# Kernel optimization log

Hardware: AMD Instinct MI355X
Metric: run time of the kernel (lower is better)

Reference implementation:

```python
import jax, jax.numpy as jnp
import numpy as np

IN_FEATURES = 4096
OUT_FEATURES = 4096
BANDWIDTH = min(IN_FEATURES, OUT_FEATURES) // 8  # 512, as in the torch default


def band_indices(n_out, n_in, bw):
    """Vectorized equivalent of BandMatrix.create_band_indices (COO row/col lists)."""
    i = np.arange(n_out)
    lo = np.maximum(0, i - bw)
    hi = np.minimum(n_in, i + bw + 1)
    counts = hi - lo
    total = int(counts.sum())
    rows = np.repeat(i, counts)
    start = np.cumsum(counts) - counts  # offset of each row's first entry
    cols = np.arange(total) - np.repeat(start, counts) + np.repeat(lo, counts)
    return rows.astype(np.int32), cols.astype(np.int32)


def setup_inputs() -> dict:
    key = jax.random.key(0)
    kx, kw = jax.random.split(key)
    rows_np, cols_np = band_indices(OUT_FEATURES, IN_FEATURES, BANDWIDTH)
    nnz = rows_np.shape[0]  # 3935744
    x = jax.random.normal(kx, (4, 2048, IN_FEATURES), dtype=jnp.float32)
    W_values = jax.random.normal(kw, (nnz,), dtype=jnp.float32)
    bias = jnp.zeros((OUT_FEATURES,), dtype=jnp.float32)
    return {
        "x": x,
        "W_values": W_values,
        "bias": bias,
        "rows": jnp.asarray(rows_np),
        "cols": jnp.asarray(cols_np),
    }


def reference(x, W_values, bias, rows, cols):
    # Densify banded COO weight [out, in] (matches sparse_coo_tensor().to_dense()).
    W = jnp.zeros((OUT_FEATURES, IN_FEATURES), dtype=W_values.dtype).at[rows, cols].set(W_values)
    # x: [B, S, in] @ W.T: [in, out] -> [B, S, out]
    out = jnp.einsum('bsi,oi->bso', x, W) + bias
    return out
```

## Files before the change

### kernel.cpp

```cpp
#include <hip/hip_runtime.h>
#include <stdint.h>

#define IN_F  4096
#define OUT_F 4096
#define BW    512
#define BM    256
#define BN    256
#define BK    32
#define WB2   1280

typedef __bf16 bf16x8 __attribute__((ext_vector_type(8)));
typedef float  f32x4  __attribute__((ext_vector_type(4)));

__device__ __forceinline__ int band_start(int o) {
    if (o <= 512)  return o * 513 + ((o * (o - 1)) >> 1);
    if (o <= 3584) return 393472 + (o - 512) * 1025;
    const int d = o - 3584;
    return 3542272 + (((1024 + 4609 - o) * d) >> 1);
}

__device__ __forceinline__ uint16_t f32_to_bf16(float f) {
    uint32_t u = __builtin_bit_cast(uint32_t, f);
    u += 0x7FFFu + ((u >> 16) & 1u);
    return (uint16_t)(u >> 16);
}

__global__ __launch_bounds__(256) void cvt_x(const float* __restrict__ x,
                                             uint16_t* __restrict__ xb, int n4) {
    const int stride = gridDim.x * 256;
    for (int i = blockIdx.x * 256 + threadIdx.x; i < n4; i += stride) {
        const float4 v = reinterpret_cast<const float4*>(x)[i];
        const uint32_t lo = (uint32_t)f32_to_bf16(v.x) | ((uint32_t)f32_to_bf16(v.y) << 16);
        const uint32_t hi = (uint32_t)f32_to_bf16(v.z) | ((uint32_t)f32_to_bf16(v.w) << 16);
        reinterpret_cast<uint2*>(xb)[i] = make_uint2(lo, hi);
    }
}

__global__ __launch_bounds__(256) void cvt_w(const float* __restrict__ wv,
                                             uint16_t* __restrict__ wd) {
    const int o = blockIdx.y;
    const int j = blockIdx.x * 256 + threadIdx.x;
    const int i = (o & ~(BM - 1)) - BW + j;
    uint16_t v = 0;
    if (i >= o - BW && i <= o + BW && i >= 0 && i < IN_F) {
        const int lo = (o > BW) ? (o - BW) : 0;
        v = f32_to_bf16(wv[band_start(o) + (i - lo)]);
    }
    wd[o * WB2 + j] = v;
}

__global__ __launch_bounds__(512, 2) void band_gemm_8p(
    const uint16_t* __restrict__ xb,
    const uint16_t* __restrict__ wd,
    const float* __restrict__ bias,
    float* __restrict__ out)
{
    __shared__ __align__(128) uint8_t lds[131072];

    const int id  = blockIdx.x;
    const int cpx = gridDim.x >> 3;
    const int wg  = (id & 7) * cpx + (id >> 3);
    const int bx  = wg & 15;
    const int by  = wg >> 4;
    const int brow = by * BM;
    const int bcol = bx * BN;

    const int wlo    = bcol - BW;
    const int kstart = wlo > 0 ? wlo : 0;
    const int kend   = (bcol + BN + BW) < IN_F ? (bcol + BN + BW) : IN_F;
    const int nt     = (kend - kstart) >> 5;
    const int j0     = kstart - wlo;

    const int tid  = threadIdx.x;
    const int w    = tid >> 6;
    const int lane = tid & 63;
    const int ln   = lane & 15;
    const int kc   = lane >> 4;
    const int wm   = w >> 2;
    const int wn   = w & 3;

    const int srow = tid >> 2;
    const int scs  = (tid & 3) ^ ((srow >> 1) & 3);
    const uint16_t* sA0 = xb + (size_t)(brow + srow) * IN_F + kstart + scs * 8;
    const uint16_t* sA1 = sA0 + (size_t)128 * IN_F;
    const uint16_t* sB0 = wd + (size_t)(bcol + srow) * WB2 + j0 + scs * 8;
    const uint16_t* sB1 = sB0 + (size_t)128 * WB2;

    const int swz  = (kc ^ ((ln >> 1) & 3)) << 4;
    const int aoff = ((wm << 7) + ln) << 6;
    const int boff = 16384 + (((wn << 6) + ln) << 6);

#define GLOAD(srcp, dst_off)                                                             \
    __builtin_amdgcn_global_load_lds(                                                    \
        (const __attribute__((address_space(1))) uint32_t*)(srcp),                       \
        (__attribute__((address_space(3))) uint32_t*)(lds + (dst_off) + (w << 10)),      \
        16, 0, 0)

    f32x4 acc[8][4] = {};

    #pragma unroll
    for (int tt = 0; tt < 3; ++tt) {
        GLOAD(sA0 + tt * 32, tt * 32768 + 0);
        GLOAD(sA1 + tt * 32, tt * 32768 + 8192);
        GLOAD(sB0 + tt * 32, tt * 32768 + 16384);
        GLOAD(sB1 + tt * 32, tt * 32768 + 24576);
    }
    asm volatile("s_waitcnt vmcnt(8)" ::: "memory");
    __builtin_amdgcn_s_barrier();

    for (int t = 0; t < nt; ++t) {
        const int cur = (t & 3) << 15;
        const int pr  = ((t + 3) & 3) << 15;
        const int ts  = (t + 3 < nt ? t + 3 : nt - 1) * 32;

        bf16x8 af[8];
        #pragma unroll
        for (int a = 0; a < 8; ++a)
            af[a] = *(const bf16x8*)(lds + cur + aoff + a * 1024 + swz);
        bf16x8 bf0 = *(const bf16x8*)(lds + cur + boff + 0 * 1024 + swz);
        bf16x8 bf1 = *(const bf16x8*)(lds + cur + boff + 1 * 1024 + swz);
        GLOAD(sA0 + ts, pr + 0);
        GLOAD(sA1 + ts, pr + 8192);
        asm volatile("" ::: "memory");
        __builtin_amdgcn_s_barrier();
        __builtin_amdgcn_s_setprio(1);
        #pragma unroll
        for (int a = 0; a < 8; ++a) {
            acc[a][0] = __builtin_amdgcn_mfma_f32_16x16x32_bf16(af[a], bf0, acc[a][0], 0, 0, 0);
            acc[a][1] = __builtin_amdgcn_mfma_f32_16x16x32_bf16(af[a], bf1, acc[a][1], 0, 0, 0);
        }
        __builtin_amdgcn_s_setprio(0);
        asm volatile("" ::: "memory");
        __builtin_amdgcn_s_barrier();

        bf16x8 bf2 = *(const bf16x8*)(lds + cur + boff + 2 * 1024 + swz);
        bf16x8 bf3 = *(const bf16x8*)(lds + cur + boff + 3 * 1024 + swz);
        GLOAD(sB0 + ts, pr + 16384);
        GLOAD(sB1 + ts, pr + 24576);
        asm volatile("s_waitcnt vmcnt(8)" ::: "memory");
        __builtin_amdgcn_s_barrier();
        __builtin_amdgcn_s_setprio(1);
        #pragma unroll
        for (int a = 0; a < 8; ++a) {
            acc[a][2] = __builtin_amdgcn_mfma_f32_16x16x32_bf16(af[a], bf2, acc[a][2], 0, 0, 0);
            acc[a][3] = __builtin_amdgcn_mfma_f32_16x16x32_bf16(af[a], bf3, acc[a][3], 0, 0, 0);
        }
        __builtin_amdgcn_s_setprio(0);
        asm volatile("" ::: "memory");
        __builtin_amdgcn_s_barrier();
    }
#undef GLOAD

    asm volatile("s_waitcnt vmcnt(0)" ::: "memory");

    const int ocol = bcol + (wn << 6) + ln;
    float bsv[4];
    #pragma unroll
    for (int b = 0; b < 4; ++b) bsv[b] = bias[ocol + b * 16];

    #pragma unroll
    for (int a = 0; a < 8; ++a) {
        #pragma unroll
        for (int q = 0; q < 4; ++q) {
            const int row = brow + (wm << 7) + a * 16 + (kc << 2) + q;
            float* po = out + (size_t)row * OUT_F + ocol;
            #pragma unroll
            for (int b = 0; b < 4; ++b)
                po[b * 16] = acc[a][b][q] + bsv[b];
        }
    }
}

__global__ __launch_bounds__(256) void band_gemm_f32(
    const float* __restrict__ x, const float* __restrict__ wv,
    const float* __restrict__ bias, float* __restrict__ out, int M)
{
    __shared__ float Xs[128][33];
    __shared__ float Ws[32][130];
    const int tid = threadIdx.x;
    const int tx = tid & 15, ty = tid >> 4;
    const int bcol = blockIdx.x * 128, brow = blockIdx.y * 128;
    const int klo = (bcol >= BW) ? (bcol - BW) : 0;
    const int khi = min(IN_F, bcol + 128 + BW);
    float acc[8][8];
    #pragma unroll
    for (int a = 0; a < 8; ++a)
        #pragma unroll
        for (int b = 0; b < 8; ++b) acc[a][b] = 0.f;
    const int xc4 = (tid & 7) * 4, xr0 = tid >> 3;
    const int wc = tid & 31, wr0 = tid >> 5;
    for (int k0 = klo; k0 < khi; k0 += 32) {
        #pragma unroll
        for (int p = 0; p < 4; ++p) {
            const int r = xr0 + 32 * p;
            const float4 v = *reinterpret_cast<const float4*>(&x[(size_t)(brow + r) * IN_F + (k0 + xc4)]);
            Xs[r][xc4 + 0] = v.x; Xs[r][xc4 + 1] = v.y; Xs[r][xc4 + 2] = v.z; Xs[r][xc4 + 3] = v.w;
        }
        const int i = k0 + wc;
        #pragma unroll
        for (int p = 0; p < 16; ++p) {
            const int r = wr0 + 8 * p;
            const int o = bcol + r;
            const int lo = (o >= BW) ? (o - BW) : 0;
            float v = 0.f;
            if (i >= o - BW && i <= o + BW) v = wv[band_start(o) + (i - lo)];
            Ws[wc][r] = v;
        }
        __syncthreads();
        #pragma unroll
        for (int k = 0; k < 32; ++k) {
            float am[8];
            #pragma unroll
            for (int a = 0; a < 8; ++a) am[a] = Xs[ty * 8 + a][k];
            float bo[8];
            #pragma unroll
            for (int b = 0; b < 4; ++b) { bo[b] = Ws[k][tx * 4 + b]; bo[4 + b] = Ws[k][tx * 4 + 64 + b]; }
            #pragma unroll
            for (int a = 0; a < 8; ++a)
                #pragma unroll
                for (int b = 0; b < 8; ++b) acc[a][b] = fmaf(am[a], bo[b], acc[a][b]);
        }
        __syncthreads();
    }
    #pragma unroll
    for (int a = 0; a < 8; ++a) {
        const size_t row = (size_t)(brow + ty * 8 + a);
        #pragma unroll
        for (int b = 0; b < 4; ++b) {
            out[row * OUT_F + bcol + tx * 4 + b]      = acc[a][b]     + bias[bcol + tx * 4 + b];
            out[row * OUT_F + bcol + tx * 4 + 64 + b] = acc[a][4 + b] + bias[bcol + tx * 4 + 64 + b];
        }
    }
}

extern "C" void kernel_launch(void* const* d_in, const int* in_sizes, int n_in,
                              void* d_out, int out_size, void* d_ws, size_t ws_size,
                              hipStream_t stream) {
    const float* x    = (const float*)d_in[0];
    const float* wv   = (const float*)d_in[1];
    const float* bias = (const float*)d_in[2];
    float* out        = (float*)d_out;

    const int M = in_sizes[0] / IN_F;
    const size_t xb_bytes = (size_t)M * IN_F * 2;
    const size_t wd_bytes = (size_t)OUT_F * WB2 * 2;

    if (ws_size >= xb_bytes + wd_bytes && (M % BM) == 0) {
        uint16_t* xb  = (uint16_t*)d_ws;
        uint16_t* wdp = (uint16_t*)((uint8_t*)d_ws + xb_bytes);
        cvt_x<<<2048, 256, 0, stream>>>(x, xb, M * IN_F / 4);
        cvt_w<<<dim3(WB2 / 256, OUT_F), 256, 0, stream>>>(wv, wdp);
        band_gemm_8p<<<(M / BM) * (OUT_F / BN), 512, 0, stream>>>(xb, wdp, bias, out);
    } else {
        dim3 grid(OUT_F / 128, M / 128);
        band_gemm_f32<<<grid, 256, 0, stream>>>(x, wv, bias, out, M);
    }
}
```

Baseline: 150.9 us.

## Retile band GEMM to 128x256 tiles with BK=64 triple-buffered pipeline

Shrinks the block tile from 256x256 to 128x256 and doubles the K step to 64, using three 48KB LDS buffers with a two-stage prefetch in place of four 32KB buffers. The grid doubles (more workgroups, 2 per CU still allowed), there are half as many K iterations per tile, and each iteration has a single barrier instead of several. It also changes the LDS swizzle to an 8-way XOR for 128-byte rows. In exchange, A-operand reuse per block drops (more weight traffic per output), and each wave holds a 4x4 accumulator set instead of 8x4.

```diff
diff --git a/kernel.cpp b/kernel.cpp
--- a/kernel.cpp
+++ b/kernel.cpp
@@ -4,10 +4,11 @@
 #define IN_F  4096
 #define OUT_F 4096
 #define BW    512
-#define BM    256
+#define TN    256
+#define WB2   1280
+#define BM    128
 #define BN    256
-#define BK    32
-#define WB2   1280
+#define BUFSZ 49152
 
 typedef __bf16 bf16x8 __attribute__((ext_vector_type(8)));
 typedef float  f32x4  __attribute__((ext_vector_type(4)));
@@ -40,7 +41,7 @@
                                              uint16_t* __restrict__ wd) {
     const int o = blockIdx.y;
     const int j = blockIdx.x * 256 + threadIdx.x;
-    const int i = (o & ~(BM - 1)) - BW + j;
+    const int i = (o & ~(TN - 1)) - BW + j;
     uint16_t v = 0;
     if (i >= o - BW && i <= o + BW && i >= 0 && i < IN_F) {
         const int lo = (o > BW) ? (o - BW) : 0;
@@ -49,13 +50,13 @@
     wd[o * WB2 + j] = v;
 }
 
-__global__ __launch_bounds__(512, 2) void band_gemm_8p(
+__global__ __launch_bounds__(512, 2) void band_gemm_v3(
     const uint16_t* __restrict__ xb,
     const uint16_t* __restrict__ wd,
     const float* __restrict__ bias,
     float* __restrict__ out)
 {
-    __shared__ __align__(128) uint8_t lds[131072];
+    __shared__ __align__(128) uint8_t lds[3 * BUFSZ];
 
     const int id  = blockIdx.x;
     const int cpx = gridDim.x >> 3;
@@ -63,12 +64,12 @@
     const int bx  = wg & 15;
     const int by  = wg >> 4;
     const int brow = by * BM;
-    const int bcol = bx * BN;
+    const int bcol = bx * TN;
 
     const int wlo    = bcol - BW;
     const int kstart = wlo > 0 ? wlo : 0;
-    const int kend   = (bcol + BN + BW) < IN_F ? (bcol + BN + BW) : IN_F;
-    const int nt     = (kend - kstart) >> 5;
+    const int kend   = (bcol + TN + BW) < IN_F ? (bcol + TN + BW) : IN_F;
+    const int nt     = (kend - kstart) >> 6;
     const int j0     = kstart - wlo;
 
     const int tid  = threadIdx.x;
@@ -79,16 +80,10 @@
     const int wm   = w >> 2;
     const int wn   = w & 3;
 
-    const int srow = tid >> 2;
-    const int scs  = (tid & 3) ^ ((srow >> 1) & 3);
-    const uint16_t* sA0 = xb + (size_t)(brow + srow) * IN_F + kstart + scs * 8;
-    const uint16_t* sA1 = sA0 + (size_t)128 * IN_F;
-    const uint16_t* sB0 = wd + (size_t)(bcol + srow) * WB2 + j0 + scs * 8;
-    const uint16_t* sB1 = sB0 + (size_t)128 * WB2;
-
-    const int swz  = (kc ^ ((ln >> 1) & 3)) << 4;
-    const int aoff = ((wm << 7) + ln) << 6;
-    const int boff = 16384 + (((wn << 6) + ln) << 6);
+    const int srow = tid >> 3;
+    const int csrc = (tid & 7) ^ (srow & 7);
+    const uint16_t* aSrc = xb + (size_t)(brow + srow) * IN_F + kstart + csrc * 8;
+    const uint16_t* bSrc = wd + (size_t)(bcol + srow) * WB2 + j0 + csrc * 8;
 
 #define GLOAD(srcp, dst_off)                                                             \
     __builtin_amdgcn_global_load_lds(                                                    \
@@ -96,73 +91,81 @@
         (__attribute__((address_space(3))) uint32_t*)(lds + (dst_off) + (w << 10)),      \
         16, 0, 0)
 
-    f32x4 acc[8][4] = {};
-
-    #pragma unroll
-    for (int tt = 0; tt < 3; ++tt) {
-        GLOAD(sA0 + tt * 32, tt * 32768 + 0);
-        GLOAD(sA1 + tt * 32, tt * 32768 + 8192);
-        GLOAD(sB0 + tt * 32, tt * 32768 + 16384);
-        GLOAD(sB1 + tt * 32, tt * 32768 + 24576);
-    }
-    asm volatile("s_waitcnt vmcnt(8)" ::: "memory");
+#define STAGE(ts_, sb_) {                                                                \
+        const uint16_t* as_ = aSrc + (ts_) * 64;                                         \
+        const uint16_t* bs_ = bSrc + (ts_) * 64;                                         \
+        GLOAD(as_,                       (sb_) + 0);                                     \
+        GLOAD(as_ + (size_t)64 * IN_F,   (sb_) + 8192);                                  \
+        GLOAD(bs_,                       (sb_) + 16384);                                 \
+        GLOAD(bs_ + (size_t)64  * WB2,   (sb_) + 24576);                                 \
+        GLOAD(bs_ + (size_t)128 * WB2,   (sb_) + 32768);                                 \
+        GLOAD(bs_ + (size_t)192 * WB2,   (sb_) + 40960); }
+
+    const int cswz = (kc ^ (ln & 7)) << 4;
+    int aOff[4], bOff[4];
+    #pragma unroll
+    for (int a = 0; a < 4; ++a) aOff[a] = ((wm * 64 + a * 16 + ln) << 7) + cswz;
+    #pragma unroll
+    for (int b = 0; b < 4; ++b) bOff[b] = 16384 + ((wn * 64 + b * 16 + ln) << 7) + cswz;
+
+    f32x4 acc[4][4] = {};
+
+    STAGE(0, 0);
+    STAGE(1, BUFSZ);
+    asm volatile("s_waitcnt vmcnt(6)" ::: "memory");
     __builtin_amdgcn_s_barrier();
 
+    int cur = 0, sb = 2 * BUFSZ;
     for (int t = 0; t < nt; ++t) {
-        const int cur = (t & 3) << 15;
-        const int pr  = ((t + 3) & 3) << 15;
-        const int ts  = (t + 3 < nt ? t + 3 : nt - 1) * 32;
-
-        bf16x8 af[8];
-        #pragma unroll
-        for (int a = 0; a < 8; ++a)
-            af[a] = *(const bf16x8*)(lds + cur + aoff + a * 1024 + swz);
-        bf16x8 bf0 = *(const bf16x8*)(lds + cur + boff + 0 * 1024 + swz);
-        bf16x8 bf1 = *(const bf16x8*)(lds + cur + boff + 1 * 1024 + swz);
-        GLOAD(sA0 + ts, pr + 0);
-        GLOAD(sA1 + ts, pr + 8192);
+        bf16x8 af0[4], bf0[4], af1[4], bf1[4];
+        #pragma unroll
+        for (int a = 0; a < 4; ++a) af0[a] = *(const bf16x8*)(lds + cur + aOff[a]);
+        #pragma unroll
+        for (int b = 0; b < 4; ++b) bf0[b] = *(const bf16x8*)(lds + cur + bOff[b]);
+
+        const bool pf = (t + 2) < nt;
+        if (pf) STAGE(t + 2, sb);
+
+        #pragma unroll
+        for (int a = 0; a < 4; ++a) af1[a] = *(const bf16x8*)(lds + cur + (aOff[a] ^ 64));
+        #pragma unroll
+        for (int b = 0; b < 4; ++b) bf1[b] = *(const bf16x8*)(lds + cur + (bOff[b] ^ 64));
+
+        __builtin_amdgcn_s_setprio(1);
+        #pragma unroll
+        for (int a = 0; a < 4; ++a)
+            #pragma unroll
+            for (int b = 0; b < 4; ++b)
+                acc[a][b] = __builtin_amdgcn_mfma_f32_16x16x32_bf16(af0[a], bf0[b], acc[a][b], 0, 0, 0);
+        #pragma unroll
+        for (int a = 0; a < 4; ++a)
+            #pragma unroll
+            for (int b = 0; b < 4; ++b)
+                acc[a][b] = __builtin_amdgcn_mfma_f32_16x16x32_bf16(af1[a], bf1[b], acc[a][b], 0, 0, 0);
+        __builtin_amdgcn_s_setprio(0);
+
+        if (pf) { asm volatile("s_waitcnt vmcnt(6)" ::: "memory"); }
+        else    { asm volatile("s_waitcnt vmcnt(0)" ::: "memory"); }
         asm volatile("" ::: "memory");
         __builtin_amdgcn_s_barrier();
-        __builtin_amdgcn_s_setprio(1);
-        #pragma unroll
-        for (int a = 0; a < 8; ++a) {
-            acc[a][0] = __builtin_amdgcn_mfma_f32_16x16x32_bf16(af[a], bf0, acc[a][0], 0, 0, 0);
-            acc[a][1] = __builtin_amdgcn_mfma_f32_16x16x32_bf16(af[a], bf1, acc[a][1], 0, 0, 0);
-        }
-        __builtin_amdgcn_s_setprio(0);
         asm volatile("" ::: "memory");
-        __builtin_amdgcn_s_barrier();
-
-        bf16x8 bf2 = *(const bf16x8*)(lds + cur + boff + 2 * 1024 + swz);
-        bf16x8 bf3 = *(const bf16x8*)(lds + cur + boff + 3 * 1024 + swz);
-        GLOAD(sB0 + ts, pr + 16384);
-        GLOAD(sB1 + ts, pr + 24576);
-        asm volatile("s_waitcnt vmcnt(8)" ::: "memory");
-        __builtin_amdgcn_s_barrier();
-        __builtin_amdgcn_s_setprio(1);
-        #pragma unroll
-        for (int a = 0; a < 8; ++a) {
-            acc[a][2] = __builtin_amdgcn_mfma_f32_16x16x32_bf16(af[a], bf2, acc[a][2], 0, 0, 0);
-            acc[a][3] = __builtin_amdgcn_mfma_f32_16x16x32_bf16(af[a], bf3, acc[a][3], 0, 0, 0);
-        }
-        __builtin_amdgcn_s_setprio(0);
-        asm volatile("" ::: "memory");
-        __builtin_amdgcn_s_barrier();
-    }
+
+        cur += BUFSZ; if (cur == 3 * BUFSZ) cur = 0;
+        sb  += BUFSZ; if (sb  == 3 * BUFSZ) sb  = 0;
+    }
+#undef STAGE
 #undef GLOAD
 
-    asm volatile("s_waitcnt vmcnt(0)" ::: "memory");
-
-    const int ocol = bcol + (wn << 6) + ln;
+    const int ocol = bcol + wn * 64 + ln;
     float bsv[4];
     #pragma unroll
     for (int b = 0; b < 4; ++b) bsv[b] = bias[ocol + b * 16];
 
     #pragma unroll
-    for (int a = 0; a < 8; ++a) {
+    for (int a = 0; a < 4; ++a) {
         #pragma unroll
         for (int q = 0; q < 4; ++q) {
-            const int row = brow + (wm << 7) + a * 16 + (kc << 2) + q;
+            const int row = brow + wm * 64 + a * 16 + (kc << 2) + q;
             float* po = out + (size_t)row * OUT_F + ocol;
             #pragma unroll
             for (int b = 0; b < 4; ++b)
@@ -250,7 +253,7 @@
         uint16_t* wdp = (uint16_t*)((uint8_t*)d_ws + xb_bytes);
         cvt_x<<<2048, 256, 0, stream>>>(x, xb, M * IN_F / 4);
         cvt_w<<<dim3(WB2 / 256, OUT_F), 256, 0, stream>>>(wv, wdp);
-        band_gemm_8p<<<(M / BM) * (OUT_F / BN), 512, 0, stream>>>(xb, wdp, bias, out);
+        band_gemm_v3<<<(M / BM) * (OUT_F / BN), 512, 0, stream>>>(xb, wdp, bias, out);
     } else {
         dim3 grid(OUT_F / 128, M / 128);
         band_gemm_f32<<<grid, 256, 0, stream>>>(x, wv, bias, out, M);
```

Result: slower. 170.2 us (+12.8%).
